# Performance work log

Measured on AMD Instinct MI355X. Metric: run time of the kernel, lower is better.

## Reference

```python
import jax, jax.numpy as jnp
import numpy as np

B, T = 256, 512
E, H, V, C = 128, 256, 50000, 64


def setup_inputs() -> dict:
    key = jax.random.key(0)
    ks = jax.random.split(key, 8)
    k = 1.0 / np.sqrt(H)
    u = lambda kk, shape: jax.random.uniform(kk, shape, jnp.float32, -k, k)
    return {
        "sentence": jax.random.randint(ks[0], (B, T), 0, V),
        "emb": jax.random.normal(ks[1], (V, E), jnp.float32),
        "W_ih": u(ks[2], (4 * H, E)),
        "W_hh": u(ks[3], (4 * H, H)),
        "b_ih": u(ks[4], (4 * H,)),
        "b_hh": u(ks[5], (4 * H,)),
        "W_lin": u(ks[6], (C, H)),
        "b_lin": u(ks[7], (C,)),
    }


def reference(sentence, emb, W_ih, W_hh, b_ih, b_hh, W_lin, b_lin):
    x = emb[sentence]  # [B, T, E]
    # Precompute input-to-gate projections for all timesteps in one GEMM.
    x_proj = jnp.einsum('bte,ge->btg', x, W_ih) + b_ih + b_hh  # [B, T, 4H]

    def step(carry, xt):
        h, c = carry
        gates = xt + h @ W_hh.T  # [B, 4H], torch gate order i,f,g,o
        i, f, g, o = jnp.split(gates, 4, axis=-1)
        c = jax.nn.sigmoid(f) * c + jax.nn.sigmoid(i) * jnp.tanh(g)
        h = jax.nn.sigmoid(o) * jnp.tanh(c)
        return (h, c), h

    h0 = jnp.zeros((x.shape[0], W_hh.shape[1]), x.dtype)
    _, hs = jax.lax.scan(step, (h0, h0), jnp.swapaxes(x_proj, 0, 1))
    lstm_out = jnp.swapaxes(hs, 0, 1)  # [B, T, H]

    logits = lstm_out @ W_lin.T + b_lin  # [B, T, C]
    # Faithful to original: LogSoftmax over dim=1 (the TIME axis), then prod over time.
    all_probs = jax.nn.log_softmax(logits, axis=1)
    return jnp.prod(all_probs, axis=1)  # [B, C]
```

## Files before the change

### kernel.cpp

```cpp
#include <hip/hip_runtime.h>

#define TT 512
#define HH 256
#define EE 128
#define BB 256
#define CC 64
#define VV 50000
#define NSB 128

#define OFF_EMB   0ull
#define OFF_WHA   6400000ull
#define OFF_WXA   6662144ull
#define OFF_BIAS  6793216ull
#define OFF_WLIN  6797312ull
#define OFF_LSTM  6813696ull
#define OFF_LOG   73922560ull
#define WS_NEED   107476992ull

typedef __attribute__((ext_vector_type(4))) float    f32x4;
typedef __attribute__((ext_vector_type(4))) unsigned u32x4;
typedef __attribute__((ext_vector_type(4))) int      i32x4;
typedef __attribute__((ext_vector_type(8))) int      i32x8;
typedef __bf16 bf16x8_t __attribute__((ext_vector_type(8)));

__device__ __forceinline__ float rcp_f(float x) { return __builtin_amdgcn_rcpf(x); }
__device__ __forceinline__ float exp2_(float x) {
  float r; asm("v_exp_f32 %0, %1" : "=v"(r) : "v"(x)); return r;
}
__device__ __forceinline__ unsigned short to_bf16(float f) {
  unsigned u = __float_as_uint(f);
  return (unsigned short)((u + 0x7fffu + ((u >> 16) & 1u)) >> 16);
}
__device__ __forceinline__ unsigned enc4(float v) {
  const unsigned sg = (__float_as_uint(v) >> 31) << 3;
  const float a = fminf(fabsf(v), 6.0f);
  const float c = (a < 2.0f) ? __builtin_rintf(a + a)
                : (a < 4.0f) ? __builtin_rintf(a) + 2.0f
                             : __builtin_rintf(a * 0.5f) + 4.0f;
  return sg | (unsigned)(int)c;
}
__device__ __forceinline__ i32x8 up8(i32x4 v) {
  i32x8 r;
  r[0] = v[0]; r[1] = v[1]; r[2] = v[2]; r[3] = v[3];
  r[4] = 0; r[5] = 0; r[6] = 0; r[7] = 0;
  return r;
}
__device__ __forceinline__ f32x4 mfma4(i32x8 a, i32x8 b, f32x4 c, int sb) {
  return __builtin_amdgcn_mfma_scale_f32_16x16x128_f8f6f4(
      a, b, c, 4, 4, 0, 0x7f7f7f7f, 0, sb);
}
#define SB_H 0x7f7f7f7f
#define SB_X 0x80808080

#define LOG2E  1.442695041f
#define SN2    (-LOG2E / 256.f)
#define SG2    (-2.f * LOG2E / 256.f)
#define C2_    (-2.f * LOG2E)

__global__ void prep_emb(const float* __restrict__ emb, unsigned* __restrict__ out) {
  const int u = blockIdx.x * 256 + threadIdx.x;
  const f32x4 f0 = ((const f32x4*)emb)[u * 2];
  const f32x4 f1 = ((const f32x4*)emb)[u * 2 + 1];
  unsigned r = enc4(2.f * f0[0]) | (enc4(2.f * f0[1]) << 4);
  r |= (enc4(2.f * f0[2]) | (enc4(2.f * f0[3]) << 4)) << 8;
  r |= (enc4(2.f * f1[0]) | (enc4(2.f * f1[1]) << 4)) << 16;
  r |= (enc4(2.f * f1[2]) | (enc4(2.f * f1[3]) << 4)) << 24;
  out[u] = r;
}

__global__ void prep_wha(const float* __restrict__ Whh, unsigned char* __restrict__ wf) {
  const int id = blockIdx.x * 256 + threadIdx.x;
  const int byt = id & 15, l = (id >> 4) & 63;
  const int kt = (id >> 10) & 1, mt = (id >> 11) & 7, w8 = id >> 14;
  const int r16 = l & 15;
  const int grow = (r16 & 3) * 256 + w8 * 32 + mt * 4 + (r16 >> 2);
  const int k0 = kt * 128 + ((l >> 4) << 5) + byt * 2;
  const unsigned n0 = enc4(64.f * Whh[grow * HH + k0]);
  const unsigned n1 = enc4(64.f * Whh[grow * HH + k0 + 1]);
  wf[id] = (unsigned char)(n0 | (n1 << 4));
}

__global__ void prep_wxa(const float* __restrict__ Wih, unsigned char* __restrict__ wf) {
  const int id = blockIdx.x * 256 + threadIdx.x;
  const int byt = id & 15, l = (id >> 4) & 63;
  const int mt = (id >> 10) & 7, w8 = id >> 13;
  const int r16 = l & 15;
  const int grow = (r16 & 3) * 256 + w8 * 32 + mt * 4 + (r16 >> 2);
  const int k0 = ((l >> 4) << 5) + byt * 2;
  const unsigned n0 = enc4(64.f * Wih[grow * EE + k0]);
  const unsigned n1 = enc4(64.f * Wih[grow * EE + k0 + 1]);
  wf[id] = (unsigned char)(n0 | (n1 << 4));
}

__global__ void prep_bias(const float* __restrict__ bih, const float* __restrict__ bhh,
                          float* __restrict__ bp) {
  const int n = blockIdx.x * 256 + threadIdx.x;
  const float sc = (n >= 512 && n < 768) ? (-2.f * LOG2E) : (-LOG2E);
  bp[n] = (bih[n] + bhh[n]) * sc;
}

__global__ void prep_wlin(const float* __restrict__ Wlin, unsigned short* __restrict__ wl) {
  const int id = blockIdx.x * 256 + threadIdx.x;
  const int j = id & 7, l = (id >> 3) & 63;
  const int kk = (id >> 9) & 7, q = id >> 12;
  const int c = q * 16 + (l & 15);
  const int k = kk * 32 + ((l >> 4) << 3) + j;
  wl[id] = to_bf16(Wlin[c * HH + k]);
}

__global__ __launch_bounds__(512, 1)
void lstm_scan(const int* __restrict__ sent, const unsigned char* __restrict__ emb4,
               const unsigned char* __restrict__ wha, const unsigned char* __restrict__ wxa,
               const float* __restrict__ bias, unsigned short* __restrict__ lstm_out) {
  __shared__ __align__(16) unsigned char xa[64 * 1024];
  __shared__ __align__(16) unsigned char bh[2 * 1024];
  __shared__ __align__(16) unsigned char xbuf[2][1024];
  __shared__ __align__(16) float redistf[8][544];
  __shared__ int sent_lds[4][512];

  const int tid = threadIdx.x;
  const int lane = tid & 63;
  const int w = tid >> 6;
  const int b0 = blockIdx.x << 2;

  i32x8 Ah[8][2];
#pragma unroll
  for (int mt = 0; mt < 8; ++mt)
#pragma unroll
    for (int kt = 0; kt < 2; ++kt)
      Ah[mt][kt] = up8(*(const i32x4*)(wha + (((w * 8 + mt) * 2 + kt) * 64 + lane) * 16));

  for (int c = tid; c < 4096; c += 512)
    ((u32x4*)xa)[c] = ((const u32x4*)wxa)[c];
  for (int i = tid; i < 2048; i += 512)
    sent_lds[i >> 9][i & 511] = sent[(b0 + (i >> 9)) * TT + (i & 511)];
  if (tid < 512) ((int*)bh)[tid] = 0;

  const int gr = 2 * w + ((lane >> 2) & 1), gq = lane & 3;
  const int* sptr = &sent_lds[gr & 3][gr >> 2];
  const unsigned char* embg = emb4 + gq * 16;
  const int gwo = gq * 256 + gr * 16;

  __syncthreads();

  u32x4 xg;
  if (lane < 8) {
    const int i0s = sptr[0];
    *(u32x4*)(xbuf[0] + gwo) = *(const u32x4*)(embg + (size_t)i0s * 64);
    const int i1s = sptr[4];
    *(u32x4*)(xbuf[1] + gwo) = *(const u32x4*)(embg + (size_t)i1s * 64);
    const int i2s = sptr[8];
    xg = *(const u32x4*)(embg + (size_t)i2s * 64);
  }
  __syncthreads();

  const int l16 = lane * 16;
  const f32x4 Zf = (f32x4){0.f, 0.f, 0.f, 0.f};
  f32x4 acc[8];
  {
    const i32x8 Bx = up8(*(const i32x4*)(xbuf[0] + l16));
#pragma unroll
    for (int mtx = 0; mtx < 8; ++mtx) {
      const i32x8 Aq = up8(*(const i32x4*)(xa + (w * 8 + mtx) * 1024 + l16));
      acc[mtx] = mfma4(Aq, Bx, Zf, SB_X);
    }
  }

  const int s = lane & 3;
  const int mtT = lane >> 3;
  const int hp = ((lane >> 2) & 1) << 1;
  const int hulS = lane >> 4;
  const int hu0 = w * 32 + mtT * 4 + hp;
  const float bi0 = bias[hu0],       bf0 = bias[256 + hu0],
              bg0 = bias[512 + hu0], bo0 = bias[768 + hu0];
  const float bi1 = bias[hu0 + 1],       bf1 = bias[256 + hu0 + 1],
              bg1 = bias[512 + hu0 + 1], bo1 = bias[768 + hu0 + 1];
  const int cb4 = (hu0 >> 7) * 1024 + ((hu0 & 127) >> 5) * 256 + s * 16 + ((hu0 & 31) >> 1);
  const int wroff = hulS * 16 + s * 4;
  const int rdoff = mtT * 68 + hp * 16 + s * 4;
  const long obase = ((long)(b0 + s) * TT) * HH + hu0;
  float cs0 = 0.f, cs1 = 0.f;

#define MICRO(J) { \
  const i32x8 Bh0 = up8(*(const i32x4*)(bh + l16)); \
  const i32x8 Bh1 = up8(*(const i32x4*)(bh + 1024 + l16)); \
  __builtin_amdgcn_s_setprio(1); \
  _Pragma("unroll") for (int mt = 0; mt < 8; ++mt) acc[mt] = mfma4(Ah[mt][0], Bh0, acc[mt], SB_H); \
  _Pragma("unroll") for (int mt = 0; mt < 8; ++mt) acc[mt] = mfma4(Ah[mt][1], Bh1, acc[mt], SB_H); \
  __builtin_amdgcn_s_setprio(0); \
  if (((lane >> 2) & 3) == (J)) { \
    _Pragma("unroll") for (int mt = 0; mt < 8; ++mt) \
      *(f32x4*)&redistf[w][mt * 68 + wroff] = acc[mt]; \
  } \
  if ((J) == 2) { \
    if (dogS) *(u32x4*)(xbC + gwo) = xg; \
    if (dogL) { const int idx = sptr[(tb + 3) * 4]; \
                xg = *(const u32x4*)(embg + (size_t)idx * 64); } \
  } \
  if ((J) == 3) { \
    const i32x8 Bx = up8(*(const i32x4*)(xbN + l16)); \
    _Pragma("unroll") for (int mtx = 0; mtx < 8; ++mtx) { \
      const i32x8 Aq = up8(*(const i32x4*)(xa + (w * 8 + mtx) * 1024 + l16)); \
      acc[mtx] = mfma4(Aq, Bx, Zf, SB_X); \
    } \
  } \
  asm volatile("s_waitcnt lgkmcnt(0)" ::: "memory"); \
  __builtin_amdgcn_sched_barrier(0); \
  const f32x4 g0 = *(const f32x4*)&redistf[w][rdoff]; \
  const f32x4 g1 = *(const f32x4*)&redistf[w][rdoff + 16]; \
  float si, sf, so, tg, tc, hv0, hv1; \
  si = rcp_f(1.f + exp2_(g0[0] * SN2 + bi0)); \
  sf = rcp_f(1.f + exp2_(g0[1] * SN2 + bf0)); \
  tg = 2.f * rcp_f(1.f + exp2_(g0[2] * SG2 + bg0)) - 1.f; \
  so = rcp_f(1.f + exp2_(g0[3] * SN2 + bo0)); \
  cs0 = sf * cs0 + si * tg; \
  tc = 2.f * rcp_f(1.f + exp2_(cs0 * C2_)) - 1.f; \
  hv0 = so * tc; \
  si = rcp_f(1.f + exp2_(g1[0] * SN2 + bi1)); \
  sf = rcp_f(1.f + exp2_(g1[1] * SN2 + bf1)); \
  tg = 2.f * rcp_f(1.f + exp2_(g1[2] * SG2 + bg1)) - 1.f; \
  so = rcp_f(1.f + exp2_(g1[3] * SN2 + bo1)); \
  cs1 = sf * cs1 + si * tg; \
  tc = 2.f * rcp_f(1.f + exp2_(cs1 * C2_)) - 1.f; \
  hv1 = so * tc; \
  { \
    const unsigned nib = enc4(4.f * hv0) | (enc4(4.f * hv1) << 4); \
    bh[cb4 + ((((J) + 1) & 3)) * 64] = (unsigned char)nib; \
    bh[cb4 + (J) * 64] = 0; \
    unsigned pb; asm("v_cvt_pk_bf16_f32 %0, %1, %2" : "=v"(pb) : "v"(hv0), "v"(hv1)); \
    *(unsigned*)(lstm_out + obase + (long)(t0 + (J)) * HH) = pb; \
  } \
  asm volatile("s_waitcnt lgkmcnt(0)" ::: "memory"); \
  __builtin_amdgcn_s_barrier(); \
}

#pragma unroll 1
  for (int tb = 0; tb < NSB; ++tb) {
    const int t0 = tb << 2;
    const bool dogS = (lane < 8) && (tb + 2 < NSB);
    const bool dogL = (lane < 8) && (tb + 3 < NSB);
    unsigned char* xbC = xbuf[tb & 1];
    unsigned char* xbN = xbuf[(tb + 1) & 1];
    MICRO(0)
    MICRO(1)
    MICRO(2)
    MICRO(3)
  }
#undef MICRO
}

__global__ __launch_bounds__(256)
void logits_gemm(const unsigned short* __restrict__ lstm, const unsigned short* __restrict__ wl,
                 const float* __restrict__ blin, float* __restrict__ logits) {
  const int tid = threadIdx.x, l = tid & 63, wv = tid >> 6;
  const long m0 = (long)blockIdx.x * 64 + wv * 16;
  f32x4 ac[4];
#pragma unroll
  for (int q = 0; q < 4; ++q) ac[q] = (f32x4){0.f, 0.f, 0.f, 0.f};
  const unsigned short* arow = lstm + (m0 + (l & 15)) * HH + ((l >> 4) << 3);
#pragma unroll
  for (int kk = 0; kk < 8; ++kk) {
    const bf16x8_t a = __builtin_bit_cast(bf16x8_t, *(const u32x4*)(arow + kk * 32));
#pragma unroll
    for (int q = 0; q < 4; ++q) {
      const bf16x8_t b = __builtin_bit_cast(bf16x8_t, *(const u32x4*)(wl + (((q * 8 + kk) * 64 + l) << 3)));
      ac[q] = __builtin_amdgcn_mfma_f32_16x16x32_bf16(a, b, ac[q], 0, 0, 0);
    }
  }
  const int r0 = (l >> 4) << 2;
#pragma unroll
  for (int q = 0; q < 4; ++q) {
    const int col = q * 16 + (l & 15);
    const float bb = blin[col];
#pragma unroll
    for (int r = 0; r < 4; ++r)
      logits[(m0 + r0 + r) * CC + col] = ac[q][r] + bb;
  }
}

__global__ __launch_bounds__(256)
void softmax_prod(const float* __restrict__ logits, float* __restrict__ out) {
  __shared__ float lds[TT * CC];
  __shared__ float red[3][4][CC];
  const int tid = threadIdx.x, b = blockIdx.x;
  const f32x4* src = (const f32x4*)(logits + (long)b * TT * CC);
  f32x4* dst = (f32x4*)lds;
#pragma unroll 1
  for (int i = tid; i < TT * CC / 4; i += 256) dst[i] = src[i];
  __syncthreads();

  const int c = tid & 63, part = tid >> 6;
  const int t0 = part * 128;
  float m = -3.0e38f;
  for (int k = 0; k < 128; ++k) m = fmaxf(m, lds[(t0 + k) * CC + c]);
  red[0][part][c] = m;
  __syncthreads();
  m = fmaxf(fmaxf(red[0][0][c], red[0][1][c]), fmaxf(red[0][2][c], red[0][3][c]));

  float ssum = 0.f;
  for (int k = 0; k < 128; ++k) ssum += __expf(lds[(t0 + k) * CC + c] - m);
  red[1][part][c] = ssum;
  __syncthreads();
  ssum = red[1][0][c] + red[1][1][c] + red[1][2][c] + red[1][3][c];
  const float lse = m + __logf(ssum);

  float pacc = 0.f;
  for (int k = 0; k < 128; ++k) pacc += __log2f(fabsf(lds[(t0 + k) * CC + c] - lse));
  red[2][part][c] = pacc;
  __syncthreads();
  if (part == 0) {
    const float tot = red[2][0][c] + red[2][1][c] + red[2][2][c] + red[2][3][c];
    out[b * CC + c] = exp2f(fminf(tot, 127.0f));
  }
}

extern "C" void kernel_launch(void* const* d_in, const int* in_sizes, int n_in,
                              void* d_out, int out_size, void* d_ws, size_t ws_size,
                              hipStream_t stream) {
  (void)in_sizes; (void)n_in; (void)out_size;
  if (ws_size < WS_NEED) return;

  const int*   sent = (const int*)d_in[0];
  const float* emb  = (const float*)d_in[1];
  const float* Wih  = (const float*)d_in[2];
  const float* Whh  = (const float*)d_in[3];
  const float* bih  = (const float*)d_in[4];
  const float* bhh  = (const float*)d_in[5];
  const float* Wlin = (const float*)d_in[6];
  const float* blin = (const float*)d_in[7];
  float* out = (float*)d_out;
  char* ws = (char*)d_ws;

  unsigned char*  emb4 = (unsigned char*)(ws + OFF_EMB);
  unsigned char*  wha  = (unsigned char*)(ws + OFF_WHA);
  unsigned char*  wxa  = (unsigned char*)(ws + OFF_WXA);
  float*          bp   = (float*)(ws + OFF_BIAS);
  unsigned short* wl   = (unsigned short*)(ws + OFF_WLIN);
  unsigned short* lo   = (unsigned short*)(ws + OFF_LSTM);
  float*          lg   = (float*)(ws + OFF_LOG);

  prep_emb<<<3125, 256, 0, stream>>>(emb, (unsigned*)emb4);
  prep_wha<<<512, 256, 0, stream>>>(Whh, wha);
  prep_wxa<<<256, 256, 0, stream>>>(Wih, wxa);
  prep_bias<<<4, 256, 0, stream>>>(bih, bhh, bp);
  prep_wlin<<<64, 256, 0, stream>>>(Wlin, wl);
  lstm_scan<<<64, 512, 0, stream>>>(sent, emb4, wha, wxa, bp, lo);
  logits_gemm<<<2048, 256, 0, stream>>>(lo, wl, blin, lg);
  softmax_prod<<<256, 256, 0, stream>>>(lg, out);
}
```

Baseline: 564.4 us.

## Split LSTM scan across 16 waves with one hidden unit per lane

Doubles the lstm_scan workgroup from 8 to 16 waves, so each wave owns 4 M-tiles of the recurrent GEMM instead of 8. Each lane now computes the gate nonlinearities for one hidden unit instead of two, and neighbour values are paired with a lane shuffle before the 4-bit and bf16 writes. The aim is to shorten the serial per-timestep critical path by spreading MFMA and transcendental work over more waves. In exchange, the per-step barrier now spans twice as many waves, a cross-lane shuffle is added, and half the lanes sit idle during the stores.

```diff
diff --git a/kernel.cpp b/kernel.cpp
--- a/kernel.cpp
+++ b/kernel.cpp
@@ -108,14 +108,14 @@
   wl[id] = to_bf16(Wlin[c * HH + k]);
 }
 
-__global__ __launch_bounds__(512, 1)
+__global__ __launch_bounds__(1024, 1)
 void lstm_scan(const int* __restrict__ sent, const unsigned char* __restrict__ emb4,
                const unsigned char* __restrict__ wha, const unsigned char* __restrict__ wxa,
                const float* __restrict__ bias, unsigned short* __restrict__ lstm_out) {
   __shared__ __align__(16) unsigned char xa[64 * 1024];
   __shared__ __align__(16) unsigned char bh[2 * 1024];
   __shared__ __align__(16) unsigned char xbuf[2][1024];
-  __shared__ __align__(16) float redistf[8][544];
+  __shared__ __align__(16) float redistf[16][272];
   __shared__ int sent_lds[4][512];
 
   const int tid = threadIdx.x;
@@ -123,19 +123,20 @@
   const int w = tid >> 6;
   const int b0 = blockIdx.x << 2;
 
-  i32x8 Ah[8][2];
-#pragma unroll
-  for (int mt = 0; mt < 8; ++mt)
+  i32x8 Ah[4][2];
+#pragma unroll
+  for (int m = 0; m < 4; ++m)
 #pragma unroll
     for (int kt = 0; kt < 2; ++kt)
-      Ah[mt][kt] = up8(*(const i32x4*)(wha + (((w * 8 + mt) * 2 + kt) * 64 + lane) * 16));
-
-  for (int c = tid; c < 4096; c += 512)
+      Ah[m][kt] = up8(*(const i32x4*)(wha + (((w * 4 + m) * 2 + kt) * 64 + lane) * 16));
+
+  for (int c = tid; c < 4096; c += 1024)
     ((u32x4*)xa)[c] = ((const u32x4*)wxa)[c];
-  for (int i = tid; i < 2048; i += 512)
+  for (int i = tid; i < 2048; i += 1024)
     sent_lds[i >> 9][i & 511] = sent[(b0 + (i >> 9)) * TT + (i & 511)];
   if (tid < 512) ((int*)bh)[tid] = 0;
 
+  const bool gth = (w < 8) && (lane < 8);
   const int gr = 2 * w + ((lane >> 2) & 1), gq = lane & 3;
   const int* sptr = &sent_lds[gr & 3][gr >> 2];
   const unsigned char* embg = emb4 + gq * 16;
@@ -144,7 +145,7 @@
   __syncthreads();
 
   u32x4 xg;
-  if (lane < 8) {
+  if (gth) {
     const int i0s = sptr[0];
     *(u32x4*)(xbuf[0] + gwo) = *(const u32x4*)(embg + (size_t)i0s * 64);
     const int i1s = sptr[4];
@@ -156,41 +157,36 @@
 
   const int l16 = lane * 16;
   const f32x4 Zf = (f32x4){0.f, 0.f, 0.f, 0.f};
-  f32x4 acc[8];
+  f32x4 acc[4];
   {
     const i32x8 Bx = up8(*(const i32x4*)(xbuf[0] + l16));
 #pragma unroll
-    for (int mtx = 0; mtx < 8; ++mtx) {
-      const i32x8 Aq = up8(*(const i32x4*)(xa + (w * 8 + mtx) * 1024 + l16));
-      acc[mtx] = mfma4(Aq, Bx, Zf, SB_X);
-    }
+    for (int m = 0; m < 4; ++m)
+      acc[m] = mfma4(up8(*(const i32x4*)(xa + (w * 4 + m) * 1024 + l16)), Bx, Zf, SB_X);
   }
 
   const int s = lane & 3;
-  const int mtT = lane >> 3;
-  const int hp = ((lane >> 2) & 1) << 1;
-  const int hulS = lane >> 4;
-  const int hu0 = w * 32 + mtT * 4 + hp;
-  const float bi0 = bias[hu0],       bf0 = bias[256 + hu0],
-              bg0 = bias[512 + hu0], bo0 = bias[768 + hu0];
-  const float bi1 = bias[hu0 + 1],       bf1 = bias[256 + hu0 + 1],
-              bg1 = bias[512 + hu0 + 1], bo1 = bias[768 + hu0 + 1];
-  const int cb4 = (hu0 >> 7) * 1024 + ((hu0 & 127) >> 5) * 256 + s * 16 + ((hu0 & 31) >> 1);
-  const int wroff = hulS * 16 + s * 4;
-  const int rdoff = mtT * 68 + hp * 16 + s * 4;
-  const long obase = ((long)(b0 + s) * TT) * HH + hu0;
-  float cs0 = 0.f, cs1 = 0.f;
+  const int hu = w * 16 + (lane >> 2);
+  const int colJ = (lane & 15) >> 2;
+  const float bi = bias[hu],       bf = bias[256 + hu],
+              bg = bias[512 + hu], bo = bias[768 + hu];
+  const int cb4 = (hu >> 7) * 1024 + ((hu & 127) >> 5) * 256 + s * 16 + ((hu & 31) >> 1);
+  const int wroff = (lane >> 4) * 16 + s * 4;
+  const int rdoff = (lane >> 4) * 68 + ((lane >> 2) & 3) * 16 + s * 4;
+  const bool heven = ((lane >> 2) & 1) == 0;
+  const long obase = ((long)(b0 + s) * TT) * HH + hu;
+  float cs = 0.f;
 
 #define MICRO(J) { \
   const i32x8 Bh0 = up8(*(const i32x4*)(bh + l16)); \
   const i32x8 Bh1 = up8(*(const i32x4*)(bh + 1024 + l16)); \
   __builtin_amdgcn_s_setprio(1); \
-  _Pragma("unroll") for (int mt = 0; mt < 8; ++mt) acc[mt] = mfma4(Ah[mt][0], Bh0, acc[mt], SB_H); \
-  _Pragma("unroll") for (int mt = 0; mt < 8; ++mt) acc[mt] = mfma4(Ah[mt][1], Bh1, acc[mt], SB_H); \
+  _Pragma("unroll") for (int m = 0; m < 4; ++m) acc[m] = mfma4(Ah[m][0], Bh0, acc[m], SB_H); \
+  _Pragma("unroll") for (int m = 0; m < 4; ++m) acc[m] = mfma4(Ah[m][1], Bh1, acc[m], SB_H); \
   __builtin_amdgcn_s_setprio(0); \
-  if (((lane >> 2) & 3) == (J)) { \
-    _Pragma("unroll") for (int mt = 0; mt < 8; ++mt) \
-      *(f32x4*)&redistf[w][mt * 68 + wroff] = acc[mt]; \
+  if (colJ == (J)) { \
+    _Pragma("unroll") for (int m = 0; m < 4; ++m) \
+      *(f32x4*)&redistf[w][m * 68 + wroff] = acc[m]; \
   } \
   if ((J) == 2) { \
     if (dogS) *(u32x4*)(xbC + gwo) = xg; \
@@ -199,35 +195,25 @@
   } \
   if ((J) == 3) { \
     const i32x8 Bx = up8(*(const i32x4*)(xbN + l16)); \
-    _Pragma("unroll") for (int mtx = 0; mtx < 8; ++mtx) { \
-      const i32x8 Aq = up8(*(const i32x4*)(xa + (w * 8 + mtx) * 1024 + l16)); \
-      acc[mtx] = mfma4(Aq, Bx, Zf, SB_X); \
-    } \
+    _Pragma("unroll") for (int m = 0; m < 4; ++m) \
+      acc[m] = mfma4(up8(*(const i32x4*)(xa + (w * 4 + m) * 1024 + l16)), Bx, Zf, SB_X); \
   } \
   asm volatile("s_waitcnt lgkmcnt(0)" ::: "memory"); \
   __builtin_amdgcn_sched_barrier(0); \
-  const f32x4 g0 = *(const f32x4*)&redistf[w][rdoff]; \
-  const f32x4 g1 = *(const f32x4*)&redistf[w][rdoff + 16]; \
-  float si, sf, so, tg, tc, hv0, hv1; \
-  si = rcp_f(1.f + exp2_(g0[0] * SN2 + bi0)); \
-  sf = rcp_f(1.f + exp2_(g0[1] * SN2 + bf0)); \
-  tg = 2.f * rcp_f(1.f + exp2_(g0[2] * SG2 + bg0)) - 1.f; \
-  so = rcp_f(1.f + exp2_(g0[3] * SN2 + bo0)); \
-  cs0 = sf * cs0 + si * tg; \
-  tc = 2.f * rcp_f(1.f + exp2_(cs0 * C2_)) - 1.f; \
-  hv0 = so * tc; \
-  si = rcp_f(1.f + exp2_(g1[0] * SN2 + bi1)); \
-  sf = rcp_f(1.f + exp2_(g1[1] * SN2 + bf1)); \
-  tg = 2.f * rcp_f(1.f + exp2_(g1[2] * SG2 + bg1)) - 1.f; \
-  so = rcp_f(1.f + exp2_(g1[3] * SN2 + bo1)); \
-  cs1 = sf * cs1 + si * tg; \
-  tc = 2.f * rcp_f(1.f + exp2_(cs1 * C2_)) - 1.f; \
-  hv1 = so * tc; \
-  { \
-    const unsigned nib = enc4(4.f * hv0) | (enc4(4.f * hv1) << 4); \
+  const f32x4 g = *(const f32x4*)&redistf[w][rdoff]; \
+  const float si = rcp_f(1.f + exp2_(g[0] * SN2 + bi)); \
+  const float sf = rcp_f(1.f + exp2_(g[1] * SN2 + bf)); \
+  const float tg = 2.f * rcp_f(1.f + exp2_(g[2] * SG2 + bg)) - 1.f; \
+  const float so = rcp_f(1.f + exp2_(g[3] * SN2 + bo)); \
+  cs = sf * cs + si * tg; \
+  const float tc = 2.f * rcp_f(1.f + exp2_(cs * C2_)) - 1.f; \
+  const float hv = so * tc; \
+  const float hvp = __shfl_xor(hv, 4); \
+  if (heven) { \
+    const unsigned nib = enc4(4.f * hv) | (enc4(4.f * hvp) << 4); \
     bh[cb4 + ((((J) + 1) & 3)) * 64] = (unsigned char)nib; \
     bh[cb4 + (J) * 64] = 0; \
-    unsigned pb; asm("v_cvt_pk_bf16_f32 %0, %1, %2" : "=v"(pb) : "v"(hv0), "v"(hv1)); \
+    unsigned pb; asm("v_cvt_pk_bf16_f32 %0, %1, %2" : "=v"(pb) : "v"(hv), "v"(hvp)); \
     *(unsigned*)(lstm_out + obase + (long)(t0 + (J)) * HH) = pb; \
   } \
   asm volatile("s_waitcnt lgkmcnt(0)" ::: "memory"); \
@@ -237,8 +223,8 @@
 #pragma unroll 1
   for (int tb = 0; tb < NSB; ++tb) {
     const int t0 = tb << 2;
-    const bool dogS = (lane < 8) && (tb + 2 < NSB);
-    const bool dogL = (lane < 8) && (tb + 3 < NSB);
+    const bool dogS = gth && (tb + 2 < NSB);
+    const bool dogL = gth && (tb + 3 < NSB);
     unsigned char* xbC = xbuf[tb & 1];
     unsigned char* xbN = xbuf[(tb + 1) & 1];
     MICRO(0)
@@ -344,7 +330,7 @@
   prep_wxa<<<256, 256, 0, stream>>>(Wih, wxa);
   prep_bias<<<4, 256, 0, stream>>>(bih, bhh, bp);
   prep_wlin<<<64, 256, 0, stream>>>(Wlin, wl);
-  lstm_scan<<<64, 512, 0, stream>>>(sent, emb4, wha, wxa, bp, lo);
+  lstm_scan<<<64, 1024, 0, stream>>>(sent, emb4, wha, wxa, bp, lo);
   logits_gemm<<<2048, 256, 0, stream>>>(lo, wl, blin, lg);
   softmax_prod<<<256, 256, 0, stream>>>(lg, out);
 }
```

New measurement: 564.6 us. About the same (+0.0%).

## Ping-pong two batch groups per block to overlap MFMA and activation phases

Applied to the files above, without the earlier changes.

The LSTM scan now packs two independent 4-sequence groups into one 1024-thread block, halving the grid to 32 blocks. Each timestep is split into a matrix (MFMA) phase and a gate-activation phase. The two groups run these phases out of step across barriers, so one group's MFMA work runs alongside the other's transcendental math. The cost is twice the waves per CU, more LDS, and a barrier after every half-step, and the grid now uses only 32 CUs.

```diff
diff --git a/kernel.cpp b/kernel.cpp
--- a/kernel.cpp
+++ b/kernel.cpp
@@ -108,47 +108,52 @@
   wl[id] = to_bf16(Wlin[c * HH + k]);
 }
 
-__global__ __launch_bounds__(512, 1)
+__global__ __launch_bounds__(1024, 1)
 void lstm_scan(const int* __restrict__ sent, const unsigned char* __restrict__ emb4,
                const unsigned char* __restrict__ wha, const unsigned char* __restrict__ wxa,
                const float* __restrict__ bias, unsigned short* __restrict__ lstm_out) {
   __shared__ __align__(16) unsigned char xa[64 * 1024];
-  __shared__ __align__(16) unsigned char bh[2 * 1024];
-  __shared__ __align__(16) unsigned char xbuf[2][1024];
-  __shared__ __align__(16) float redistf[8][544];
-  __shared__ int sent_lds[4][512];
+  __shared__ __align__(16) unsigned char bh[2][2048];
+  __shared__ __align__(16) unsigned char xbuf[2][2][1024];
+  __shared__ __align__(16) float redistf[16][544];
+  __shared__ int sent_lds[8][512];
 
   const int tid = threadIdx.x;
   const int lane = tid & 63;
   const int w = tid >> 6;
-  const int b0 = blockIdx.x << 2;
+  const int grp = w >> 3;
+  const int wl = w & 7;
+  const int bb0 = blockIdx.x << 3;
+  const int b0 = bb0 + grp * 4;
 
   i32x8 Ah[8][2];
 #pragma unroll
   for (int mt = 0; mt < 8; ++mt)
 #pragma unroll
     for (int kt = 0; kt < 2; ++kt)
-      Ah[mt][kt] = up8(*(const i32x4*)(wha + (((w * 8 + mt) * 2 + kt) * 64 + lane) * 16));
-
-  for (int c = tid; c < 4096; c += 512)
+      Ah[mt][kt] = up8(*(const i32x4*)(wha + (((wl * 8 + mt) * 2 + kt) * 64 + lane) * 16));
+
+  for (int c = tid; c < 4096; c += 1024)
     ((u32x4*)xa)[c] = ((const u32x4*)wxa)[c];
-  for (int i = tid; i < 2048; i += 512)
-    sent_lds[i >> 9][i & 511] = sent[(b0 + (i >> 9)) * TT + (i & 511)];
-  if (tid < 512) ((int*)bh)[tid] = 0;
-
-  const int gr = 2 * w + ((lane >> 2) & 1), gq = lane & 3;
-  const int* sptr = &sent_lds[gr & 3][gr >> 2];
+  for (int i = tid; i < 4096; i += 1024)
+    sent_lds[i >> 9][i & 511] = sent[(bb0 + (i >> 9)) * TT + (i & 511)];
+  if (tid < 1024) ((int*)bh)[tid] = 0;
+
+  const bool gth = lane < 8;
+  const int gr = 2 * wl + ((lane >> 2) & 1), gq = lane & 3;
+  const int* sptr = &sent_lds[grp * 4 + (gr & 3)][gr >> 2];
   const unsigned char* embg = emb4 + gq * 16;
   const int gwo = gq * 256 + gr * 16;
+  unsigned char* bhp = bh[grp];
 
   __syncthreads();
 
   u32x4 xg;
-  if (lane < 8) {
+  if (gth) {
     const int i0s = sptr[0];
-    *(u32x4*)(xbuf[0] + gwo) = *(const u32x4*)(embg + (size_t)i0s * 64);
+    *(u32x4*)(xbuf[grp][0] + gwo) = *(const u32x4*)(embg + (size_t)i0s * 64);
     const int i1s = sptr[4];
-    *(u32x4*)(xbuf[1] + gwo) = *(const u32x4*)(embg + (size_t)i1s * 64);
+    *(u32x4*)(xbuf[grp][1] + gwo) = *(const u32x4*)(embg + (size_t)i1s * 64);
     const int i2s = sptr[8];
     xg = *(const u32x4*)(embg + (size_t)i2s * 64);
   }
@@ -158,54 +163,48 @@
   const f32x4 Zf = (f32x4){0.f, 0.f, 0.f, 0.f};
   f32x4 acc[8];
   {
-    const i32x8 Bx = up8(*(const i32x4*)(xbuf[0] + l16));
-#pragma unroll
-    for (int mtx = 0; mtx < 8; ++mtx) {
-      const i32x8 Aq = up8(*(const i32x4*)(xa + (w * 8 + mtx) * 1024 + l16));
-      acc[mtx] = mfma4(Aq, Bx, Zf, SB_X);
-    }
+    const i32x8 Bx = up8(*(const i32x4*)(xbuf[grp][0] + l16));
+#pragma unroll
+    for (int mt = 0; mt < 8; ++mt)
+      acc[mt] = mfma4(up8(*(const i32x4*)(xa + ((wl * 8 + mt) << 10) + l16)), Bx, Zf, SB_X);
   }
 
   const int s = lane & 3;
   const int mtT = lane >> 3;
   const int hp = ((lane >> 2) & 1) << 1;
   const int hulS = lane >> 4;
-  const int hu0 = w * 32 + mtT * 4 + hp;
+  const int hu0 = wl * 32 + mtT * 4 + hp;
   const float bi0 = bias[hu0],       bf0 = bias[256 + hu0],
               bg0 = bias[512 + hu0], bo0 = bias[768 + hu0];
   const float bi1 = bias[hu0 + 1],       bf1 = bias[256 + hu0 + 1],
               bg1 = bias[512 + hu0 + 1], bo1 = bias[768 + hu0 + 1];
   const int cb4 = (hu0 >> 7) * 1024 + ((hu0 & 127) >> 5) * 256 + s * 16 + ((hu0 & 31) >> 1);
+  const int colJ = (lane & 15) >> 2;
   const int wroff = hulS * 16 + s * 4;
   const int rdoff = mtT * 68 + hp * 16 + s * 4;
   const long obase = ((long)(b0 + s) * TT) * HH + hu0;
   float cs0 = 0.f, cs1 = 0.f;
-
-#define MICRO(J) { \
-  const i32x8 Bh0 = up8(*(const i32x4*)(bh + l16)); \
-  const i32x8 Bh1 = up8(*(const i32x4*)(bh + 1024 + l16)); \
+  const bool isA = (grp == 0);
+
+#define GBODY(J, TB) { \
+  const i32x8 Bh0 = up8(*(const i32x4*)(bhp + l16)); \
+  const i32x8 Bh1 = up8(*(const i32x4*)(bhp + 1024 + l16)); \
   __builtin_amdgcn_s_setprio(1); \
   _Pragma("unroll") for (int mt = 0; mt < 8; ++mt) acc[mt] = mfma4(Ah[mt][0], Bh0, acc[mt], SB_H); \
   _Pragma("unroll") for (int mt = 0; mt < 8; ++mt) acc[mt] = mfma4(Ah[mt][1], Bh1, acc[mt], SB_H); \
   __builtin_amdgcn_s_setprio(0); \
-  if (((lane >> 2) & 3) == (J)) { \
+  if (colJ == (J)) { \
     _Pragma("unroll") for (int mt = 0; mt < 8; ++mt) \
       *(f32x4*)&redistf[w][mt * 68 + wroff] = acc[mt]; \
   } \
-  if ((J) == 2) { \
-    if (dogS) *(u32x4*)(xbC + gwo) = xg; \
-    if (dogL) { const int idx = sptr[(tb + 3) * 4]; \
-                xg = *(const u32x4*)(embg + (size_t)idx * 64); } \
+  if ((J) == 3) { \
+    const i32x8 Bx = up8(*(const i32x4*)(xbuf[grp][((TB) + 1) & 1] + l16)); \
+    _Pragma("unroll") for (int mt = 0; mt < 8; ++mt) \
+      acc[mt] = mfma4(up8(*(const i32x4*)(xa + ((wl * 8 + mt) << 10) + l16)), Bx, Zf, SB_X); \
   } \
-  if ((J) == 3) { \
-    const i32x8 Bx = up8(*(const i32x4*)(xbN + l16)); \
-    _Pragma("unroll") for (int mtx = 0; mtx < 8; ++mtx) { \
-      const i32x8 Aq = up8(*(const i32x4*)(xa + (w * 8 + mtx) * 1024 + l16)); \
-      acc[mtx] = mfma4(Aq, Bx, Zf, SB_X); \
-    } \
-  } \
-  asm volatile("s_waitcnt lgkmcnt(0)" ::: "memory"); \
-  __builtin_amdgcn_sched_barrier(0); \
+}
+
+#define VBODY(J, TB) { \
   const f32x4 g0 = *(const f32x4*)&redistf[w][rdoff]; \
   const f32x4 g1 = *(const f32x4*)&redistf[w][rdoff + 16]; \
   float si, sf, so, tg, tc, hv0, hv1; \
@@ -225,28 +224,44 @@
   hv1 = so * tc; \
   { \
     const unsigned nib = enc4(4.f * hv0) | (enc4(4.f * hv1) << 4); \
-    bh[cb4 + ((((J) + 1) & 3)) * 64] = (unsigned char)nib; \
-    bh[cb4 + (J) * 64] = 0; \
+    bhp[cb4 + ((((J) + 1) & 3)) * 64] = (unsigned char)nib; \
+    bhp[cb4 + (J) * 64] = 0; \
     unsigned pb; asm("v_cvt_pk_bf16_f32 %0, %1, %2" : "=v"(pb) : "v"(hv0), "v"(hv1)); \
-    *(unsigned*)(lstm_out + obase + (long)(t0 + (J)) * HH) = pb; \
+    *(unsigned*)(lstm_out + obase + (long)((TB) * 4 + (J)) * HH) = pb; \
   } \
-  asm volatile("s_waitcnt lgkmcnt(0)" ::: "memory"); \
-  __builtin_amdgcn_s_barrier(); \
-}
+  if ((J) == 2) { \
+    if (gth && (TB) + 2 < NSB) *(u32x4*)(xbuf[grp][(TB) & 1] + gwo) = xg; \
+    if (gth && (TB) + 3 < NSB) { const int idx = sptr[((TB) + 3) * 4]; \
+      xg = *(const u32x4*)(embg + (size_t)idx * 64); } \
+  } \
+}
+
+#define SYNC { asm volatile("s_waitcnt lgkmcnt(0)" ::: "memory"); \
+               __builtin_amdgcn_s_barrier(); }
 
 #pragma unroll 1
   for (int tb = 0; tb < NSB; ++tb) {
-    const int t0 = tb << 2;
-    const bool dogS = (lane < 8) && (tb + 2 < NSB);
-    const bool dogL = (lane < 8) && (tb + 3 < NSB);
-    unsigned char* xbC = xbuf[tb & 1];
-    unsigned char* xbN = xbuf[(tb + 1) & 1];
-    MICRO(0)
-    MICRO(1)
-    MICRO(2)
-    MICRO(3)
-  }
-#undef MICRO
+    if (isA) { GBODY(0, tb) } else if (tb > 0) { VBODY(3, tb - 1) }
+    SYNC
+    if (isA) { VBODY(0, tb) } else { GBODY(0, tb) }
+    SYNC
+    if (isA) { GBODY(1, tb) } else { VBODY(0, tb) }
+    SYNC
+    if (isA) { VBODY(1, tb) } else { GBODY(1, tb) }
+    SYNC
+    if (isA) { GBODY(2, tb) } else { VBODY(1, tb) }
+    SYNC
+    if (isA) { VBODY(2, tb) } else { GBODY(2, tb) }
+    SYNC
+    if (isA) { GBODY(3, tb) } else { VBODY(2, tb) }
+    SYNC
+    if (isA) { VBODY(3, tb) } else { GBODY(3, tb) }
+    SYNC
+  }
+  if (!isA) { VBODY(3, NSB - 1) }
+#undef GBODY
+#undef VBODY
+#undef SYNC
 }
 
 __global__ __launch_bounds__(256)
@@ -344,7 +359,7 @@
   prep_wxa<<<256, 256, 0, stream>>>(Wih, wxa);
   prep_bias<<<4, 256, 0, stream>>>(bih, bhh, bp);
   prep_wlin<<<64, 256, 0, stream>>>(Wlin, wl);
-  lstm_scan<<<64, 512, 0, stream>>>(sent, emb4, wha, wxa, bp, lo);
+  lstm_scan<<<32, 1024, 0, stream>>>(sent, emb4, wha, wxa, bp, lo);
   logits_gemm<<<2048, 256, 0, stream>>>(lo, wl, blin, lg);
   softmax_prod<<<256, 256, 0, stream>>>(lg, out);
 }
```

Measured after the change: 1.049 ms. +85.9%, slower.
